# Kernel tuning notes

Hardware: AMD Instinct MI355X
Metric: run time of the kernel (lower is better)

## Reference

```python
import jax, jax.numpy as jnp
import numpy as np

B = 4096
D1 = 2048   # APPEARANCE_DIM
D2 = 1024   # POSE_DIM
DF = 8192   # FUSED_DIM
LN_EPS = 1e-5
L2_EPS = 1e-12


def setup_inputs() -> dict:
    key = jax.random.key(0)
    ks = jax.random.split(key, 6)
    x = jax.random.normal(ks[0], (B, D1), dtype=jnp.float32)
    y = jax.random.normal(ks[1], (B, D2), dtype=jnp.float32)
    h1 = jax.random.randint(ks[2], (D1,), 0, DF, dtype=jnp.int32)
    h2 = jax.random.randint(ks[3], (D2,), 0, DF, dtype=jnp.int32)
    s1 = (2 * jax.random.randint(ks[4], (D1,), 0, 2) - 1).astype(jnp.float32)
    s2 = (2 * jax.random.randint(ks[5], (D2,), 0, 2) - 1).astype(jnp.float32)
    gamma = jnp.ones((DF,), dtype=jnp.float32)
    beta = jnp.zeros((DF,), dtype=jnp.float32)
    return {"x": x, "y": y, "s1": s1, "s2": s2, "gamma": gamma,
            "beta": beta, "h1": h1, "h2": h2}


def count_sketch(v, h, s, out_dim):
    # v: [B, Din], h: [Din] int indices into out_dim, s: [Din] +-1 signs
    # single vectorized scatter-add along the feature axis
    return jnp.zeros((v.shape[0], out_dim), v.dtype).at[:, h].add(v * s)


def reference(x, y, s1, s2, gamma, beta, h1, h2):
    x_sk = count_sketch(x, h1, s1, DF)          # [B, DF]
    y_sk = count_sketch(y, h2, s2, DF)          # [B, DF]
    # circular convolution via FFT
    fused = jnp.fft.ifft(jnp.fft.fft(x_sk, axis=1) * jnp.fft.fft(y_sk, axis=1),
                         axis=1).real           # [B, DF]
    # LayerNorm over last dim
    mu = jnp.mean(fused, axis=-1, keepdims=True)
    var = jnp.mean(jnp.square(fused - mu), axis=-1, keepdims=True)
    normed = (fused - mu) * jax.lax.rsqrt(var + LN_EPS) * gamma + beta
    # F.normalize(p=2, dim=1)
    nrm = jnp.linalg.norm(normed, axis=1, keepdims=True)
    return normed / jnp.maximum(nrm, L2_EPS)
```

## Files before the change

kernel.cpp:

```cpp
#include <hip/hip_runtime.h>
#include <math.h>

#define DF 8192
#define NT 512

#define PH(i) ((i) ^ (((i) >> 5) & 14))

__device__ __forceinline__ float2 cmul(float2 a, float2 b) {
    return make_float2(a.x * b.x - a.y * b.y, a.x * b.y + a.y * b.x);
}
__device__ __forceinline__ float2 cadd(float2 a, float2 b) { return make_float2(a.x + b.x, a.y + b.y); }
__device__ __forceinline__ float2 csub(float2 a, float2 b) { return make_float2(a.x - b.x, a.y - b.y); }
__device__ __forceinline__ float2 cmuli(float2 a) { return make_float2(-a.y, a.x); }

#define RT_C 0.92387953251128674f
#define RT_S 0.38268343236508977f
#define RT_H 0.70710678118654752f

__device__ __forceinline__ float2 rootF(int j) {
    switch (j & 7) {
        case 0:  return make_float2( 1.f,   0.f  );
        case 1:  return make_float2( RT_C, -RT_S );
        case 2:  return make_float2( RT_H, -RT_H );
        case 3:  return make_float2( RT_S, -RT_C );
        case 4:  return make_float2( 0.f,  -1.f  );
        case 5:  return make_float2(-RT_S, -RT_C );
        case 6:  return make_float2(-RT_H, -RT_H );
        default: return make_float2(-RT_C, -RT_S );
    }
}
__device__ __forceinline__ float2 rootI(int j) {
    float2 r = rootF(j);
    return make_float2(r.x, -r.y);
}

__device__ __forceinline__ int brev9(int x) { return (int)(__brev((unsigned)x) >> 23); }

__device__ __forceinline__ void fft16_dif(float2 v[16], float2 wb) {
    const float2 wb2 = cmul(wb, wb);
    const float2 wb4 = cmul(wb2, wb2);
    const float2 wb8 = cmul(wb4, wb4);
    #pragma unroll
    for (int m = 0; m < 8; ++m) {
        float2 W = cmul(wb, rootF(m));
        float2 a = v[m], b = v[m + 8];
        v[m] = cadd(a, b);
        v[m + 8] = cmul(csub(a, b), W);
    }
    #pragma unroll
    for (int g = 0; g < 2; ++g)
        #pragma unroll
        for (int m = 0; m < 4; ++m) {
            int i = 8 * g + m;
            float2 W = cmul(wb2, rootF(2 * m));
            float2 a = v[i], b = v[i + 4];
            v[i] = cadd(a, b);
            v[i + 4] = cmul(csub(a, b), W);
        }
    #pragma unroll
    for (int g = 0; g < 4; ++g)
        #pragma unroll
        for (int m = 0; m < 2; ++m) {
            int i = 4 * g + m;
            float2 W = cmul(wb4, rootF(4 * m));
            float2 a = v[i], b = v[i + 2];
            v[i] = cadd(a, b);
            v[i + 2] = cmul(csub(a, b), W);
        }
    #pragma unroll
    for (int g = 0; g < 8; ++g) {
        int i = 2 * g;
        float2 a = v[i], b = v[i + 1];
        v[i] = cadd(a, b);
        v[i + 1] = cmul(csub(a, b), wb8);
    }
}

__device__ __forceinline__ void bf_dit(float2& a, float2& b, float2 W) {
    float2 bw = cmul(b, W);
    float2 ta = a;
    a = cadd(ta, bw);
    b = csub(ta, bw);
}
__device__ __forceinline__ void bf_dit1(float2& a, float2& b) {
    float2 tb = b, ta = a;
    a = cadd(ta, tb);
    b = csub(ta, tb);
}
__device__ __forceinline__ void bf_diti(float2& a, float2& b) {
    float2 bw = cmuli(b);
    float2 ta = a;
    a = cadd(ta, bw);
    b = csub(ta, bw);
}

__device__ __forceinline__ void fft8_dit(float2 v[8], float2 wq) {
    const float2 wq2 = cmul(wq, wq);
    const float2 wq4 = cmul(wq2, wq2);
    #pragma unroll
    for (int g = 0; g < 4; ++g) bf_dit(v[2 * g], v[2 * g + 1], wq4);
    #pragma unroll
    for (int g = 0; g < 2; ++g) {
        bf_dit(v[4 * g],     v[4 * g + 2], wq2);
        bf_dit(v[4 * g + 1], v[4 * g + 3], cmuli(wq2));
    }
    bf_dit(v[0], v[4], wq);
    bf_dit(v[1], v[5], cmul(wq, make_float2(RT_H, RT_H)));
    bf_dit(v[2], v[6], cmuli(wq));
    bf_dit(v[3], v[7], cmul(wq, make_float2(-RT_H, RT_H)));
}

__device__ __forceinline__ void fft8_dit1(float2 v[8]) {
    #pragma unroll
    for (int g = 0; g < 4; ++g) bf_dit1(v[2 * g], v[2 * g + 1]);
    #pragma unroll
    for (int g = 0; g < 2; ++g) {
        bf_dit1(v[4 * g],     v[4 * g + 2]);
        bf_diti(v[4 * g + 1], v[4 * g + 3]);
    }
    bf_dit1(v[0], v[4]);
    bf_dit (v[1], v[5], make_float2(RT_H, RT_H));
    bf_diti(v[2], v[6]);
    bf_dit (v[3], v[7], make_float2(-RT_H, RT_H));
}

__global__ __launch_bounds__(NT, 4)
void mcb3(const float* __restrict__ x, const float* __restrict__ y,
          const float* __restrict__ s1, const float* __restrict__ s2,
          const float* __restrict__ gamma, const float* __restrict__ beta,
          const int* __restrict__ h1, const int* __restrict__ h2,
          float* __restrict__ out)
{
    __shared__ float2 z[DF];
    const int t = threadIdx.x;
    const int row = blockIdx.x;

    #pragma unroll
    for (int m = 0; m < 16; ++m) z[t + NT * m] = make_float2(0.f, 0.f);
    __syncthreads();

    {
        const float4* x4  = (const float4*)(x + (size_t)row * 2048);
        const float4* s14 = (const float4*)s1;
        const int4*   h14 = (const int4*)h1;
        float4 xv = x4[t], sv = s14[t];
        int4 hv = h14[t];
        atomicAdd(&z[PH(hv.x)].x, xv.x * sv.x);
        atomicAdd(&z[PH(hv.y)].x, xv.y * sv.y);
        atomicAdd(&z[PH(hv.z)].x, xv.z * sv.z);
        atomicAdd(&z[PH(hv.w)].x, xv.w * sv.w);
        const float2* y2  = (const float2*)(y + (size_t)row * 1024);
        const float2* s22 = (const float2*)s2;
        const int2*   h22 = (const int2*)h2;
        float2 yv = y2[t], tv = s22[t];
        int2 hw = h22[t];
        atomicAdd(&z[PH(hw.x)].y, yv.x * tv.x);
        atomicAdd(&z[PH(hw.y)].y, yv.y * tv.y);
    }
    __syncthreads();

    float sn, cs;

    {
        float2 v[16];
        #pragma unroll
        for (int m = 0; m < 16; ++m) v[m] = z[PH(t + 512 * m)];
        __sincosf(-(float)M_PI / 4096.f * (float)t, &sn, &cs);
        fft16_dif(v, make_float2(cs, sn));
        #pragma unroll
        for (int m = 0; m < 16; ++m) z[PH(t + 512 * m)] = v[m];
    }
    __syncthreads();

    {
        const int lo = t & 31, hi = t >> 5;
        float2 v[16];
        #pragma unroll
        for (int m = 0; m < 16; ++m) v[m] = z[PH(lo + 32 * m + 512 * hi)];
        __sincosf(-(float)M_PI / 256.f * (float)lo, &sn, &cs);
        fft16_dif(v, make_float2(cs, sn));
        #pragma unroll
        for (int m = 0; m < 16; ++m) z[PH(lo + 32 * m + 512 * hi)] = v[m];
    }
    __syncthreads();

    {
        const int lo = t & 1, hi = t >> 1;
        float2 v[16];
        #pragma unroll
        for (int m = 0; m < 16; ++m) v[m] = z[PH(lo + 2 * m + 32 * hi)];
        __sincosf(-(float)M_PI / 16.f * (float)lo, &sn, &cs);
        fft16_dif(v, make_float2(cs, sn));
        #pragma unroll
        for (int m = 0; m < 16; ++m) z[PH(lo + 2 * m + 32 * hi)] = v[m];
    }
    __syncthreads();

    float2 u8[8];
    {
        const int R  = brev9(t);
        const int tp = brev9((512 - R) & 511);
        float2 a[8], b[8], pa[8], pb[8];
        #pragma unroll
        for (int m = 0; m < 8; ++m) {
            float4 q = *(const float4*)&z[PH(16 * t + 2 * m)];
            a[m] = make_float2(q.x, q.y);  b[m] = make_float2(q.z, q.w);
            float4 qp = *(const float4*)&z[PH(16 * tp + 2 * (7 - m))];
            pa[m] = make_float2(qp.x, qp.y); pb[m] = make_float2(qp.z, qp.w);
        }
        #pragma unroll
        for (int m = 0; m < 8; ++m) {
            float2 ta = a[m],  tb = b[m];
            a[m] = cadd(ta, tb);  b[m] = csub(ta, tb);
            ta = pa[m]; tb = pb[m];
            pa[m] = cadd(ta, tb); pb[m] = csub(ta, tb);
        }
        if (t == 0) {
            float2 ca[8], cb[8];
            #pragma unroll
            for (int m = 0; m < 8; ++m) { ca[m] = a[m]; cb[m] = b[m]; }
            const int tbl[8] = {0, 1, 3, 2, 7, 6, 5, 4};
            #pragma unroll
            for (int m = 0; m < 8; ++m) {
                if (m == 0) { pa[0] = cb[0]; pb[0] = ca[0]; }
                else        { pa[m] = ca[tbl[m]]; pb[m] = cb[tbl[m]]; }
            }
        }
        __sincosf((float)M_PI / 4096.f * (float)R, &sn, &cs);
        const float2 wR = make_float2(cs, sn);
        const float invN = 1.f / 8192.f;
        const int MB[8] = {0, 4, 2, 6, 1, 5, 3, 7};
        #pragma unroll
        for (int m = 0; m < 8; ++m) {
            float2 A = a[m], B = b[m], A2 = pa[m], B2 = pb[m];
            float X1r = 0.5f * (A.x + B2.x), X1i = 0.5f * (A.y - B2.y);
            float Y1r = 0.5f * (A.y + B2.y), Y1i = 0.5f * (B2.x - A.x);
            float2 P1 = make_float2((X1r * Y1r - X1i * Y1i) * invN,
                                    (X1r * Y1i + X1i * Y1r) * invN);
            float X2r = 0.5f * (B.x + A2.x), X2i = 0.5f * (B.y - A2.y);
            float Y2r = 0.5f * (B.y + A2.y), Y2i = 0.5f * (A2.x - B.x);
            float2 P2 = make_float2((X2r * Y2r - X2i * Y2i) * invN,
                                    (X2r * Y2i + X2i * Y2r) * invN);
            float2 S = cadd(P1, P2);
            float2 D = csub(P1, P2);
            float2 Dw = cmul(D, cmul(wR, rootI(MB[m])));
            u8[m] = make_float2(S.x - Dw.y, S.y + Dw.x);
        }
        fft8_dit1(u8);
        __syncthreads();
        #pragma unroll
        for (int g = 0; g < 4; ++g) {
            *(float4*)&z[PH(8 * t + 2 * g)] =
                make_float4(u8[2 * g].x, u8[2 * g].y, u8[2 * g + 1].x, u8[2 * g + 1].y);
        }
    }
    __syncthreads();

    {
        const int lo = t & 7, hi = t >> 3;
        #pragma unroll
        for (int m = 0; m < 8; ++m) u8[m] = z[PH(lo + 8 * m + 64 * hi)];
        __sincosf((float)M_PI / 32.f * (float)lo, &sn, &cs);
        fft8_dit(u8, make_float2(cs, sn));
        #pragma unroll
        for (int m = 0; m < 8; ++m) z[PH(lo + 8 * m + 64 * hi)] = u8[m];
    }
    __syncthreads();

    {
        const int lo = t & 63, hi = t >> 6;
        #pragma unroll
        for (int m = 0; m < 8; ++m) u8[m] = z[PH(lo + 64 * m + 512 * hi)];
        __sincosf((float)M_PI / 256.f * (float)lo, &sn, &cs);
        fft8_dit(u8, make_float2(cs, sn));
        #pragma unroll
        for (int m = 0; m < 8; ++m) z[PH(lo + 64 * m + 512 * hi)] = u8[m];
    }
    __syncthreads();

    #pragma unroll
    for (int m = 0; m < 8; ++m) u8[m] = z[PH(t + 512 * m)];
    __sincosf((float)M_PI / 2048.f * (float)t, &sn, &cs);
    fft8_dit(u8, make_float2(cs, sn));

    float lsum = 0.f, lsq = 0.f;
    #pragma unroll
    for (int m = 0; m < 8; ++m) {
        lsum += u8[m].x + u8[m].y;
        lsq  += u8[m].x * u8[m].x + u8[m].y * u8[m].y;
    }
    #pragma unroll
    for (int k = 32; k >= 1; k >>= 1) { lsum += __shfl_xor(lsum, k); lsq += __shfl_xor(lsq, k); }
    const int wid = t >> 6, lane = t & 63;
    __syncthreads();
    if (lane == 0) z[wid] = make_float2(lsum, lsq);
    __syncthreads();
    float tsum = 0.f, tsq = 0.f;
    #pragma unroll
    for (int w = 0; w < 8; ++w) { tsum += z[w].x; tsq += z[w].y; }
    const float mu   = tsum * (1.f / (float)DF);
    const float var  = tsq * (1.f / (float)DF) - mu * mu;
    const float rstd = rsqrtf(var + 1e-5f);

    const float2* g2  = (const float2*)gamma;
    const float2* bt2 = (const float2*)beta;
    float2 nv[8];
    float lsq2 = 0.f;
    #pragma unroll
    for (int m = 0; m < 8; ++m) {
        int i = t + 512 * m;
        float2 g = g2[i], bb = bt2[i];
        float ne = (u8[m].x - mu) * rstd * g.x + bb.x;
        float no = (u8[m].y - mu) * rstd * g.y + bb.y;
        nv[m] = make_float2(ne, no);
        lsq2 += ne * ne + no * no;
    }
    #pragma unroll
    for (int k = 32; k >= 1; k >>= 1) lsq2 += __shfl_xor(lsq2, k);
    if (lane == 0) z[8 + wid].x = lsq2;
    __syncthreads();
    float t2 = 0.f;
    #pragma unroll
    for (int w = 0; w < 8; ++w) t2 += z[8 + w].x;
    const float inv = 1.f / fmaxf(sqrtf(t2), 1e-12f);

    float2* o2 = (float2*)(out + (size_t)row * DF);
    #pragma unroll
    for (int m = 0; m < 8; ++m)
        o2[t + 512 * m] = make_float2(nv[m].x * inv, nv[m].y * inv);
}

extern "C" void kernel_launch(void* const* d_in, const int* in_sizes, int n_in,
                              void* d_out, int out_size, void* d_ws, size_t ws_size,
                              hipStream_t stream) {
    const float* x     = (const float*)d_in[0];
    const float* y     = (const float*)d_in[1];
    const float* s1    = (const float*)d_in[2];
    const float* s2    = (const float*)d_in[3];
    const float* gamma = (const float*)d_in[4];
    const float* beta  = (const float*)d_in[5];
    const int*   h1    = (const int*)d_in[6];
    const int*   h2    = (const int*)d_in[7];
    float* out = (float*)d_out;

    hipLaunchKernelGGL(mcb3, dim3(4096), dim3(NT), 0, stream,
                       x, y, s1, s2, gamma, beta, h1, h2, out);
}
```

Measured before the change: 180.3 us.

## Process two rows per block to amortize twiddles and syncs

Each block now handles two batch rows with a 128 KB shared buffer, interleaving the two FFT pipelines so twiddle computation, index math, hash/sign loads and barriers are shared across rows. This doubles the independent work per thread, which raises ILP and halves the grid. In exchange, shared memory and register use per block double and launch bounds drop to 2 blocks per CU, which may reduce occupancy and latency hiding.

```diff
diff --git a/kernel.cpp b/kernel.cpp
--- a/kernel.cpp
+++ b/kernel.cpp
@@ -36,298 +36,303 @@
 
 __device__ __forceinline__ int brev9(int x) { return (int)(__brev((unsigned)x) >> 23); }
 
-__device__ __forceinline__ void fft16_dif(float2 v[16], float2 wb) {
+__device__ __forceinline__ void bf_dif_dual(float2& a0, float2& b0, float2& a1, float2& b1, float2 W) {
+    float2 d0 = csub(a0, b0); a0 = cadd(a0, b0); b0 = cmul(d0, W);
+    float2 d1 = csub(a1, b1); a1 = cadd(a1, b1); b1 = cmul(d1, W);
+}
+__device__ __forceinline__ void bf_dit_dual(float2& a0, float2& b0, float2& a1, float2& b1, float2 W) {
+    float2 w0 = cmul(b0, W); b0 = csub(a0, w0); a0 = cadd(a0, w0);
+    float2 w1 = cmul(b1, W); b1 = csub(a1, w1); a1 = cadd(a1, w1);
+}
+__device__ __forceinline__ void bf_dit1_dual(float2& a0, float2& b0, float2& a1, float2& b1) {
+    float2 t0 = b0; b0 = csub(a0, t0); a0 = cadd(a0, t0);
+    float2 t1 = b1; b1 = csub(a1, t1); a1 = cadd(a1, t1);
+}
+__device__ __forceinline__ void bf_diti_dual(float2& a0, float2& b0, float2& a1, float2& b1) {
+    float2 w0 = cmuli(b0); b0 = csub(a0, w0); a0 = cadd(a0, w0);
+    float2 w1 = cmuli(b1); b1 = csub(a1, w1); a1 = cadd(a1, w1);
+}
+
+__device__ __forceinline__ void fft16_dif_dual(float2 va[16], float2 vb[16], float2 wb) {
     const float2 wb2 = cmul(wb, wb);
     const float2 wb4 = cmul(wb2, wb2);
     const float2 wb8 = cmul(wb4, wb4);
     #pragma unroll
     for (int m = 0; m < 8; ++m) {
         float2 W = cmul(wb, rootF(m));
-        float2 a = v[m], b = v[m + 8];
-        v[m] = cadd(a, b);
-        v[m + 8] = cmul(csub(a, b), W);
-    }
-    #pragma unroll
-    for (int g = 0; g < 2; ++g)
-        #pragma unroll
-        for (int m = 0; m < 4; ++m) {
-            int i = 8 * g + m;
-            float2 W = cmul(wb2, rootF(2 * m));
-            float2 a = v[i], b = v[i + 4];
-            v[i] = cadd(a, b);
-            v[i + 4] = cmul(csub(a, b), W);
+        bf_dif_dual(va[m], va[m + 8], vb[m], vb[m + 8], W);
+    }
+    #pragma unroll
+    for (int m = 0; m < 4; ++m) {
+        float2 W = cmul(wb2, rootF(2 * m));
+        bf_dif_dual(va[m],     va[m + 4],  vb[m],     vb[m + 4],  W);
+        bf_dif_dual(va[8 + m], va[12 + m], vb[8 + m], vb[12 + m], W);
+    }
+    #pragma unroll
+    for (int m = 0; m < 2; ++m) {
+        float2 W = cmul(wb4, rootF(4 * m));
+        #pragma unroll
+        for (int g = 0; g < 4; ++g) {
+            int i = 4 * g + m;
+            bf_dif_dual(va[i], va[i + 2], vb[i], vb[i + 2], W);
         }
-    #pragma unroll
-    for (int g = 0; g < 4; ++g)
-        #pragma unroll
-        for (int m = 0; m < 2; ++m) {
-            int i = 4 * g + m;
-            float2 W = cmul(wb4, rootF(4 * m));
-            float2 a = v[i], b = v[i + 2];
-            v[i] = cadd(a, b);
-            v[i + 2] = cmul(csub(a, b), W);
-        }
-    #pragma unroll
-    for (int g = 0; g < 8; ++g) {
-        int i = 2 * g;
-        float2 a = v[i], b = v[i + 1];
-        v[i] = cadd(a, b);
-        v[i + 1] = cmul(csub(a, b), wb8);
-    }
-}
-
-__device__ __forceinline__ void bf_dit(float2& a, float2& b, float2 W) {
-    float2 bw = cmul(b, W);
-    float2 ta = a;
-    a = cadd(ta, bw);
-    b = csub(ta, bw);
-}
-__device__ __forceinline__ void bf_dit1(float2& a, float2& b) {
-    float2 tb = b, ta = a;
-    a = cadd(ta, tb);
-    b = csub(ta, tb);
-}
-__device__ __forceinline__ void bf_diti(float2& a, float2& b) {
-    float2 bw = cmuli(b);
-    float2 ta = a;
-    a = cadd(ta, bw);
-    b = csub(ta, bw);
-}
-
-__device__ __forceinline__ void fft8_dit(float2 v[8], float2 wq) {
+    }
+    #pragma unroll
+    for (int g = 0; g < 8; ++g)
+        bf_dif_dual(va[2 * g], va[2 * g + 1], vb[2 * g], vb[2 * g + 1], wb8);
+}
+
+__device__ __forceinline__ void fft8_dit_dual(float2 va[8], float2 vb[8], float2 wq) {
     const float2 wq2 = cmul(wq, wq);
     const float2 wq4 = cmul(wq2, wq2);
     #pragma unroll
-    for (int g = 0; g < 4; ++g) bf_dit(v[2 * g], v[2 * g + 1], wq4);
+    for (int g = 0; g < 4; ++g) bf_dit_dual(va[2 * g], va[2 * g + 1], vb[2 * g], vb[2 * g + 1], wq4);
+    const float2 iwq2 = cmuli(wq2);
     #pragma unroll
     for (int g = 0; g < 2; ++g) {
-        bf_dit(v[4 * g],     v[4 * g + 2], wq2);
-        bf_dit(v[4 * g + 1], v[4 * g + 3], cmuli(wq2));
-    }
-    bf_dit(v[0], v[4], wq);
-    bf_dit(v[1], v[5], cmul(wq, make_float2(RT_H, RT_H)));
-    bf_dit(v[2], v[6], cmuli(wq));
-    bf_dit(v[3], v[7], cmul(wq, make_float2(-RT_H, RT_H)));
-}
-
-__device__ __forceinline__ void fft8_dit1(float2 v[8]) {
-    #pragma unroll
-    for (int g = 0; g < 4; ++g) bf_dit1(v[2 * g], v[2 * g + 1]);
+        bf_dit_dual(va[4 * g],     va[4 * g + 2], vb[4 * g],     vb[4 * g + 2], wq2);
+        bf_dit_dual(va[4 * g + 1], va[4 * g + 3], vb[4 * g + 1], vb[4 * g + 3], iwq2);
+    }
+    bf_dit_dual(va[0], va[4], vb[0], vb[4], wq);
+    bf_dit_dual(va[1], va[5], vb[1], vb[5], cmul(wq, make_float2(RT_H, RT_H)));
+    bf_dit_dual(va[2], va[6], vb[2], vb[6], cmuli(wq));
+    bf_dit_dual(va[3], va[7], vb[3], vb[7], cmul(wq, make_float2(-RT_H, RT_H)));
+}
+__device__ __forceinline__ void fft8_dit1_dual(float2 va[8], float2 vb[8]) {
+    #pragma unroll
+    for (int g = 0; g < 4; ++g) bf_dit1_dual(va[2 * g], va[2 * g + 1], vb[2 * g], vb[2 * g + 1]);
     #pragma unroll
     for (int g = 0; g < 2; ++g) {
-        bf_dit1(v[4 * g],     v[4 * g + 2]);
-        bf_diti(v[4 * g + 1], v[4 * g + 3]);
-    }
-    bf_dit1(v[0], v[4]);
-    bf_dit (v[1], v[5], make_float2(RT_H, RT_H));
-    bf_diti(v[2], v[6]);
-    bf_dit (v[3], v[7], make_float2(-RT_H, RT_H));
-}
-
-__global__ __launch_bounds__(NT, 4)
-void mcb3(const float* __restrict__ x, const float* __restrict__ y,
+        bf_dit1_dual(va[4 * g],     va[4 * g + 2], vb[4 * g],     vb[4 * g + 2]);
+        bf_diti_dual(va[4 * g + 1], va[4 * g + 3], vb[4 * g + 1], vb[4 * g + 3]);
+    }
+    bf_dit1_dual(va[0], va[4], vb[0], vb[4]);
+    bf_dit_dual (va[1], va[5], vb[1], vb[5], make_float2(RT_H, RT_H));
+    bf_diti_dual(va[2], va[6], vb[2], vb[6]);
+    bf_dit_dual (va[3], va[7], vb[3], vb[7], make_float2(-RT_H, RT_H));
+}
+
+__device__ __forceinline__ float2 mega_combine(float2 A, float2 B, float2 PA, float2 PB,
+                                               float2 W, float invN) {
+    float X1r = 0.5f * (A.x + PB.x), X1i = 0.5f * (A.y - PB.y);
+    float Y1r = 0.5f * (A.y + PB.y), Y1i = 0.5f * (PB.x - A.x);
+    float2 P1 = make_float2((X1r * Y1r - X1i * Y1i) * invN, (X1r * Y1i + X1i * Y1r) * invN);
+    float X2r = 0.5f * (B.x + PA.x), X2i = 0.5f * (B.y - PA.y);
+    float Y2r = 0.5f * (B.y + PA.y), Y2i = 0.5f * (PA.x - B.x);
+    float2 P2 = make_float2((X2r * Y2r - X2i * Y2i) * invN, (X2r * Y2i + X2i * Y2r) * invN);
+    float2 S = cadd(P1, P2);
+    float2 D = csub(P1, P2);
+    float2 Dw = cmul(D, W);
+    return make_float2(S.x - Dw.y, S.y + Dw.x);
+}
+
+__global__ __launch_bounds__(NT, 2)
+void mcb4(const float* __restrict__ x, const float* __restrict__ y,
           const float* __restrict__ s1, const float* __restrict__ s2,
           const float* __restrict__ gamma, const float* __restrict__ beta,
           const int* __restrict__ h1, const int* __restrict__ h2,
           float* __restrict__ out)
 {
-    __shared__ float2 z[DF];
+    __shared__ float2 z[2 * DF];
+    float2* z0 = z;
+    float2* z1 = z + DF;
     const int t = threadIdx.x;
-    const int row = blockIdx.x;
-
-    #pragma unroll
-    for (int m = 0; m < 16; ++m) z[t + NT * m] = make_float2(0.f, 0.f);
-    __syncthreads();
-
-    {
-        const float4* x4  = (const float4*)(x + (size_t)row * 2048);
-        const float4* s14 = (const float4*)s1;
-        const int4*   h14 = (const int4*)h1;
-        float4 xv = x4[t], sv = s14[t];
-        int4 hv = h14[t];
-        atomicAdd(&z[PH(hv.x)].x, xv.x * sv.x);
-        atomicAdd(&z[PH(hv.y)].x, xv.y * sv.y);
-        atomicAdd(&z[PH(hv.z)].x, xv.z * sv.z);
-        atomicAdd(&z[PH(hv.w)].x, xv.w * sv.w);
-        const float2* y2  = (const float2*)(y + (size_t)row * 1024);
-        const float2* s22 = (const float2*)s2;
-        const int2*   h22 = (const int2*)h2;
-        float2 yv = y2[t], tv = s22[t];
-        int2 hw = h22[t];
-        atomicAdd(&z[PH(hw.x)].y, yv.x * tv.x);
-        atomicAdd(&z[PH(hw.y)].y, yv.y * tv.y);
+    const int rA = blockIdx.x * 2, rB = rA + 1;
+
+    {
+        float4* z4 = (float4*)z;
+        #pragma unroll
+        for (int m = 0; m < 16; ++m) z4[t + NT * m] = make_float4(0.f, 0.f, 0.f, 0.f);
+    }
+    __syncthreads();
+
+    {
+        float4 sv = ((const float4*)s1)[t];
+        int4   hv = ((const int4*)h1)[t];
+        float4 xa = ((const float4*)(x + (size_t)rA * 2048))[t];
+        float4 xb = ((const float4*)(x + (size_t)rB * 2048))[t];
+        int p0 = PH(hv.x), p1 = PH(hv.y), p2 = PH(hv.z), p3 = PH(hv.w);
+        atomicAdd(&z0[p0].x, xa.x * sv.x);  atomicAdd(&z1[p0].x, xb.x * sv.x);
+        atomicAdd(&z0[p1].x, xa.y * sv.y);  atomicAdd(&z1[p1].x, xb.y * sv.y);
+        atomicAdd(&z0[p2].x, xa.z * sv.z);  atomicAdd(&z1[p2].x, xb.z * sv.z);
+        atomicAdd(&z0[p3].x, xa.w * sv.w);  atomicAdd(&z1[p3].x, xb.w * sv.w);
+        float2 tv = ((const float2*)s2)[t];
+        int2   hw = ((const int2*)h2)[t];
+        float2 ya = ((const float2*)(y + (size_t)rA * 1024))[t];
+        float2 yb = ((const float2*)(y + (size_t)rB * 1024))[t];
+        int q0 = PH(hw.x), q1 = PH(hw.y);
+        atomicAdd(&z0[q0].y, ya.x * tv.x);  atomicAdd(&z1[q0].y, yb.x * tv.x);
+        atomicAdd(&z0[q1].y, ya.y * tv.y);  atomicAdd(&z1[q1].y, yb.y * tv.y);
     }
     __syncthreads();
 
     float sn, cs;
-
-    {
-        float2 v[16];
-        #pragma unroll
-        for (int m = 0; m < 16; ++m) v[m] = z[PH(t + 512 * m)];
+    {
+        float2 va[16], vb[16];
+
+        #pragma unroll
+        for (int m = 0; m < 16; ++m) { int p = PH(t + 512 * m); va[m] = z0[p]; vb[m] = z1[p]; }
         __sincosf(-(float)M_PI / 4096.f * (float)t, &sn, &cs);
-        fft16_dif(v, make_float2(cs, sn));
-        #pragma unroll
-        for (int m = 0; m < 16; ++m) z[PH(t + 512 * m)] = v[m];
-    }
-    __syncthreads();
-
-    {
-        const int lo = t & 31, hi = t >> 5;
-        float2 v[16];
-        #pragma unroll
-        for (int m = 0; m < 16; ++m) v[m] = z[PH(lo + 32 * m + 512 * hi)];
-        __sincosf(-(float)M_PI / 256.f * (float)lo, &sn, &cs);
-        fft16_dif(v, make_float2(cs, sn));
-        #pragma unroll
-        for (int m = 0; m < 16; ++m) z[PH(lo + 32 * m + 512 * hi)] = v[m];
-    }
-    __syncthreads();
-
-    {
-        const int lo = t & 1, hi = t >> 1;
-        float2 v[16];
-        #pragma unroll
-        for (int m = 0; m < 16; ++m) v[m] = z[PH(lo + 2 * m + 32 * hi)];
-        __sincosf(-(float)M_PI / 16.f * (float)lo, &sn, &cs);
-        fft16_dif(v, make_float2(cs, sn));
-        #pragma unroll
-        for (int m = 0; m < 16; ++m) z[PH(lo + 2 * m + 32 * hi)] = v[m];
-    }
-    __syncthreads();
-
-    float2 u8[8];
+        fft16_dif_dual(va, vb, make_float2(cs, sn));
+        #pragma unroll
+        for (int m = 0; m < 16; ++m) { int p = PH(t + 512 * m); z0[p] = va[m]; z1[p] = vb[m]; }
+        __syncthreads();
+
+        {
+            const int lo = t & 31, hi = t >> 5;
+            #pragma unroll
+            for (int m = 0; m < 16; ++m) { int p = PH(lo + 32 * m + 512 * hi); va[m] = z0[p]; vb[m] = z1[p]; }
+            __sincosf(-(float)M_PI / 256.f * (float)lo, &sn, &cs);
+            fft16_dif_dual(va, vb, make_float2(cs, sn));
+            #pragma unroll
+            for (int m = 0; m < 16; ++m) { int p = PH(lo + 32 * m + 512 * hi); z0[p] = va[m]; z1[p] = vb[m]; }
+        }
+        __syncthreads();
+
+        {
+            const int lo = t & 1, hi = t >> 1;
+            #pragma unroll
+            for (int m = 0; m < 16; ++m) { int p = PH(lo + 2 * m + 32 * hi); va[m] = z0[p]; vb[m] = z1[p]; }
+            __sincosf(-(float)M_PI / 16.f * (float)lo, &sn, &cs);
+            fft16_dif_dual(va, vb, make_float2(cs, sn));
+            #pragma unroll
+            for (int m = 0; m < 16; ++m) { int p = PH(lo + 2 * m + 32 * hi); z0[p] = va[m]; z1[p] = vb[m]; }
+        }
+        __syncthreads();
+    }
+
+    float2 uA[8], uB[8];
     {
         const int R  = brev9(t);
         const int tp = brev9((512 - R) & 511);
-        float2 a[8], b[8], pa[8], pb[8];
-        #pragma unroll
-        for (int m = 0; m < 8; ++m) {
-            float4 q = *(const float4*)&z[PH(16 * t + 2 * m)];
-            a[m] = make_float2(q.x, q.y);  b[m] = make_float2(q.z, q.w);
-            float4 qp = *(const float4*)&z[PH(16 * tp + 2 * (7 - m))];
-            pa[m] = make_float2(qp.x, qp.y); pb[m] = make_float2(qp.z, qp.w);
-        }
-        #pragma unroll
-        for (int m = 0; m < 8; ++m) {
-            float2 ta = a[m],  tb = b[m];
-            a[m] = cadd(ta, tb);  b[m] = csub(ta, tb);
-            ta = pa[m]; tb = pb[m];
-            pa[m] = cadd(ta, tb); pb[m] = csub(ta, tb);
-        }
-        if (t == 0) {
-            float2 ca[8], cb[8];
-            #pragma unroll
-            for (int m = 0; m < 8; ++m) { ca[m] = a[m]; cb[m] = b[m]; }
-            const int tbl[8] = {0, 1, 3, 2, 7, 6, 5, 4};
-            #pragma unroll
-            for (int m = 0; m < 8; ++m) {
-                if (m == 0) { pa[0] = cb[0]; pb[0] = ca[0]; }
-                else        { pa[m] = ca[tbl[m]]; pb[m] = cb[tbl[m]]; }
-            }
-        }
         __sincosf((float)M_PI / 4096.f * (float)R, &sn, &cs);
         const float2 wR = make_float2(cs, sn);
         const float invN = 1.f / 8192.f;
-        const int MB[8] = {0, 4, 2, 6, 1, 5, 3, 7};
+        const int MB[8]   = {0, 4, 2, 6, 1, 5, 3, 7};
+        const int TBL2[8] = {0, 2, 6, 4, 14, 12, 10, 8};
         #pragma unroll
         for (int m = 0; m < 8; ++m) {
-            float2 A = a[m], B = b[m], A2 = pa[m], B2 = pb[m];
-            float X1r = 0.5f * (A.x + B2.x), X1i = 0.5f * (A.y - B2.y);
-            float Y1r = 0.5f * (A.y + B2.y), Y1i = 0.5f * (B2.x - A.x);
-            float2 P1 = make_float2((X1r * Y1r - X1i * Y1i) * invN,
-                                    (X1r * Y1i + X1i * Y1r) * invN);
-            float X2r = 0.5f * (B.x + A2.x), X2i = 0.5f * (B.y - A2.y);
-            float Y2r = 0.5f * (B.y + A2.y), Y2i = 0.5f * (A2.x - B.x);
-            float2 P2 = make_float2((X2r * Y2r - X2i * Y2i) * invN,
-                                    (X2r * Y2i + X2i * Y2r) * invN);
-            float2 S = cadd(P1, P2);
-            float2 D = csub(P1, P2);
-            float2 Dw = cmul(D, cmul(wR, rootI(MB[m])));
-            u8[m] = make_float2(S.x - Dw.y, S.y + Dw.x);
+            int own = PH(16 * t + 2 * m);
+            int pp  = (t == 0) ? PH(TBL2[m]) : PH(16 * tp + 2 * (7 - m));
+            float4 qa = *(const float4*)&z0[own];
+            float4 qb = *(const float4*)&z1[own];
+            float4 ra = *(const float4*)&z0[pp];
+            float4 rb = *(const float4*)&z1[pp];
+            float2 A0  = make_float2(qa.x + qa.z, qa.y + qa.w);
+            float2 B0  = make_float2(qa.x - qa.z, qa.y - qa.w);
+            float2 A1  = make_float2(qb.x + qb.z, qb.y + qb.w);
+            float2 B1  = make_float2(qb.x - qb.z, qb.y - qb.w);
+            float2 PA0 = make_float2(ra.x + ra.z, ra.y + ra.w);
+            float2 PB0 = make_float2(ra.x - ra.z, ra.y - ra.w);
+            float2 PA1 = make_float2(rb.x + rb.z, rb.y + rb.w);
+            float2 PB1 = make_float2(rb.x - rb.z, rb.y - rb.w);
+            if (m == 0) {
+                if (t == 0) {
+                    float2 s0 = PA0; PA0 = PB0; PB0 = s0;
+                    float2 s1_ = PA1; PA1 = PB1; PB1 = s1_;
+                }
+            }
+            float2 W = cmul(wR, rootI(MB[m]));
+            uA[m] = mega_combine(A0, B0, PA0, PB0, W, invN);
+            uB[m] = mega_combine(A1, B1, PA1, PB1, W, invN);
         }
-        fft8_dit1(u8);
-        __syncthreads();
-        #pragma unroll
-        for (int g = 0; g < 4; ++g) {
-            *(float4*)&z[PH(8 * t + 2 * g)] =
-                make_float4(u8[2 * g].x, u8[2 * g].y, u8[2 * g + 1].x, u8[2 * g + 1].y);
-        }
+        fft8_dit1_dual(uA, uB);
+    }
+    __syncthreads();
+    #pragma unroll
+    for (int g = 0; g < 4; ++g) {
+        int p = PH(8 * t + 2 * g);
+        *(float4*)&z0[p] = make_float4(uA[2 * g].x, uA[2 * g].y, uA[2 * g + 1].x, uA[2 * g + 1].y);
+        *(float4*)&z1[p] = make_float4(uB[2 * g].x, uB[2 * g].y, uB[2 * g + 1].x, uB[2 * g + 1].y);
     }
     __syncthreads();
 
     {
         const int lo = t & 7, hi = t >> 3;
         #pragma unroll
-        for (int m = 0; m < 8; ++m) u8[m] = z[PH(lo + 8 * m + 64 * hi)];
+        for (int m = 0; m < 8; ++m) { int p = PH(lo + 8 * m + 64 * hi); uA[m] = z0[p]; uB[m] = z1[p]; }
         __sincosf((float)M_PI / 32.f * (float)lo, &sn, &cs);
-        fft8_dit(u8, make_float2(cs, sn));
-        #pragma unroll
-        for (int m = 0; m < 8; ++m) z[PH(lo + 8 * m + 64 * hi)] = u8[m];
+        fft8_dit_dual(uA, uB, make_float2(cs, sn));
+        #pragma unroll
+        for (int m = 0; m < 8; ++m) { int p = PH(lo + 8 * m + 64 * hi); z0[p] = uA[m]; z1[p] = uB[m]; }
     }
     __syncthreads();
 
     {
         const int lo = t & 63, hi = t >> 6;
         #pragma unroll
-        for (int m = 0; m < 8; ++m) u8[m] = z[PH(lo + 64 * m + 512 * hi)];
+        for (int m = 0; m < 8; ++m) { int p = PH(lo + 64 * m + 512 * hi); uA[m] = z0[p]; uB[m] = z1[p]; }
         __sincosf((float)M_PI / 256.f * (float)lo, &sn, &cs);
-        fft8_dit(u8, make_float2(cs, sn));
-        #pragma unroll
-        for (int m = 0; m < 8; ++m) z[PH(lo + 64 * m + 512 * hi)] = u8[m];
-    }
-    __syncthreads();
-
-    #pragma unroll
-    for (int m = 0; m < 8; ++m) u8[m] = z[PH(t + 512 * m)];
+        fft8_dit_dual(uA, uB, make_float2(cs, sn));
+        #pragma unroll
+        for (int m = 0; m < 8; ++m) { int p = PH(lo + 64 * m + 512 * hi); z0[p] = uA[m]; z1[p] = uB[m]; }
+    }
+    __syncthreads();
+
+    #pragma unroll
+    for (int m = 0; m < 8; ++m) { int p = PH(t + 512 * m); uA[m] = z0[p]; uB[m] = z1[p]; }
     __sincosf((float)M_PI / 2048.f * (float)t, &sn, &cs);
-    fft8_dit(u8, make_float2(cs, sn));
-
-    float lsum = 0.f, lsq = 0.f;
+    fft8_dit_dual(uA, uB, make_float2(cs, sn));
+
+    float lsA = 0.f, lqA = 0.f, lsB = 0.f, lqB = 0.f;
     #pragma unroll
     for (int m = 0; m < 8; ++m) {
-        lsum += u8[m].x + u8[m].y;
-        lsq  += u8[m].x * u8[m].x + u8[m].y * u8[m].y;
-    }
-    #pragma unroll
-    for (int k = 32; k >= 1; k >>= 1) { lsum += __shfl_xor(lsum, k); lsq += __shfl_xor(lsq, k); }
+        lsA += uA[m].x + uA[m].y;  lqA += uA[m].x * uA[m].x + uA[m].y * uA[m].y;
+        lsB += uB[m].x + uB[m].y;  lqB += uB[m].x * uB[m].x + uB[m].y * uB[m].y;
+    }
+    #pragma unroll
+    for (int k = 32; k >= 1; k >>= 1) {
+        lsA += __shfl_xor(lsA, k);  lqA += __shfl_xor(lqA, k);
+        lsB += __shfl_xor(lsB, k);  lqB += __shfl_xor(lqB, k);
+    }
     const int wid = t >> 6, lane = t & 63;
     __syncthreads();
-    if (lane == 0) z[wid] = make_float2(lsum, lsq);
-    __syncthreads();
-    float tsum = 0.f, tsq = 0.f;
-    #pragma unroll
-    for (int w = 0; w < 8; ++w) { tsum += z[w].x; tsq += z[w].y; }
-    const float mu   = tsum * (1.f / (float)DF);
-    const float var  = tsq * (1.f / (float)DF) - mu * mu;
-    const float rstd = rsqrtf(var + 1e-5f);
+    if (lane == 0) { z0[wid] = make_float2(lsA, lqA); z1[wid] = make_float2(lsB, lqB); }
+    __syncthreads();
+    float tsA = 0.f, tqA = 0.f, tsB = 0.f, tqB = 0.f;
+    #pragma unroll
+    for (int w = 0; w < 8; ++w) {
+        tsA += z0[w].x; tqA += z0[w].y;
+        tsB += z1[w].x; tqB += z1[w].y;
+    }
+    const float muA = tsA * (1.f / (float)DF);
+    const float muB = tsB * (1.f / (float)DF);
+    const float rstdA = rsqrtf(tqA * (1.f / (float)DF) - muA * muA + 1e-5f);
+    const float rstdB = rsqrtf(tqB * (1.f / (float)DF) - muB * muB + 1e-5f);
 
     const float2* g2  = (const float2*)gamma;
     const float2* bt2 = (const float2*)beta;
-    float2 nv[8];
-    float lsq2 = 0.f;
+    float l2A = 0.f, l2B = 0.f;
     #pragma unroll
     for (int m = 0; m < 8; ++m) {
         int i = t + 512 * m;
         float2 g = g2[i], bb = bt2[i];
-        float ne = (u8[m].x - mu) * rstd * g.x + bb.x;
-        float no = (u8[m].y - mu) * rstd * g.y + bb.y;
-        nv[m] = make_float2(ne, no);
-        lsq2 += ne * ne + no * no;
-    }
-    #pragma unroll
-    for (int k = 32; k >= 1; k >>= 1) lsq2 += __shfl_xor(lsq2, k);
-    if (lane == 0) z[8 + wid].x = lsq2;
-    __syncthreads();
-    float t2 = 0.f;
-    #pragma unroll
-    for (int w = 0; w < 8; ++w) t2 += z[8 + w].x;
-    const float inv = 1.f / fmaxf(sqrtf(t2), 1e-12f);
-
-    float2* o2 = (float2*)(out + (size_t)row * DF);
-    #pragma unroll
-    for (int m = 0; m < 8; ++m)
-        o2[t + 512 * m] = make_float2(nv[m].x * inv, nv[m].y * inv);
+        float aE = (uA[m].x - muA) * rstdA * g.x + bb.x;
+        float aO = (uA[m].y - muA) * rstdA * g.y + bb.y;
+        float bE = (uB[m].x - muB) * rstdB * g.x + bb.x;
+        float bO = (uB[m].y - muB) * rstdB * g.y + bb.y;
+        uA[m] = make_float2(aE, aO);
+        uB[m] = make_float2(bE, bO);
+        l2A += aE * aE + aO * aO;
+        l2B += bE * bE + bO * bO;
+    }
+    #pragma unroll
+    for (int k = 32; k >= 1; k >>= 1) { l2A += __shfl_xor(l2A, k); l2B += __shfl_xor(l2B, k); }
+    if (lane == 0) z0[8 + wid] = make_float2(l2A, l2B);
+    __syncthreads();
+    float t2A = 0.f, t2B = 0.f;
+    #pragma unroll
+    for (int w = 0; w < 8; ++w) { t2A += z0[8 + w].x; t2B += z0[8 + w].y; }
+    const float invA = 1.f / fmaxf(sqrtf(t2A), 1e-12f);
+    const float invB = 1.f / fmaxf(sqrtf(t2B), 1e-12f);
+
+    float2* oA = (float2*)(out + (size_t)rA * DF);
+    float2* oB = (float2*)(out + (size_t)rB * DF);
+    #pragma unroll
+    for (int m = 0; m < 8; ++m) {
+        oA[t + 512 * m] = make_float2(uA[m].x * invA, uA[m].y * invA);
+        oB[t + 512 * m] = make_float2(uB[m].x * invB, uB[m].y * invB);
+    }
 }
 
 extern "C" void kernel_launch(void* const* d_in, const int* in_sizes, int n_in,
@@ -343,6 +348,6 @@
     const int*   h2    = (const int*)d_in[7];
     float* out = (float*)d_out;
 
-    hipLaunchKernelGGL(mcb3, dim3(4096), dim3(NT), 0, stream,
+    hipLaunchKernelGGL(mcb4, dim3(2048), dim3(NT), 0, stream,
                        x, y, s1, s2, gamma, beta, h1, h2, out);
 }
```

Result: slower. 211.3 us (+17.2%).

## Restructure FFT passes into wave-local stages with wave-level sync instead of block barriers

Applied to the files above, without the earlier changes.

Reorganizes the forward FFT middle stages so each wavefront owns a contiguous 1024-element chunk (radix-8 plus radix-16 plus radix-4 sub-stages). This lets block-wide __syncthreads be replaced by s_waitcnt wave-level waits, and the inverse FFT middle stages get the same treatment. The pair-combine step now reads partner values directly from LDS inside the loop rather than preloading them, which lowers register pressure. The swizzle also widens to reduce bank conflicts. Relying on lgkmcnt waits alone for intra-wave LDS ordering is riskier than full barriers.

```diff
diff --git a/kernel.cpp b/kernel.cpp
--- a/kernel.cpp
+++ b/kernel.cpp
@@ -4,14 +4,17 @@
 #define DF 8192
 #define NT 512
 
-#define PH(i) ((i) ^ (((i) >> 5) & 14))
+#define SW(i) ((i) ^ (((i) >> 5) & 30))
+
+#define WAVE_SYNC asm volatile("s_waitcnt lgkmcnt(0)" ::: "memory")
 
 __device__ __forceinline__ float2 cmul(float2 a, float2 b) {
     return make_float2(a.x * b.x - a.y * b.y, a.x * b.y + a.y * b.x);
 }
 __device__ __forceinline__ float2 cadd(float2 a, float2 b) { return make_float2(a.x + b.x, a.y + b.y); }
 __device__ __forceinline__ float2 csub(float2 a, float2 b) { return make_float2(a.x - b.x, a.y - b.y); }
-__device__ __forceinline__ float2 cmuli(float2 a) { return make_float2(-a.y, a.x); }
+__device__ __forceinline__ float2 cmuli(float2 a)  { return make_float2(-a.y, a.x); }
+__device__ __forceinline__ float2 cmulmi(float2 a) { return make_float2(a.y, -a.x); }
 
 #define RT_C 0.92387953251128674f
 #define RT_S 0.38268343236508977f
@@ -36,46 +39,21 @@
 
 __device__ __forceinline__ int brev9(int x) { return (int)(__brev((unsigned)x) >> 23); }
 
-__device__ __forceinline__ void fft16_dif(float2 v[16], float2 wb) {
-    const float2 wb2 = cmul(wb, wb);
-    const float2 wb4 = cmul(wb2, wb2);
-    const float2 wb8 = cmul(wb4, wb4);
-    #pragma unroll
-    for (int m = 0; m < 8; ++m) {
-        float2 W = cmul(wb, rootF(m));
-        float2 a = v[m], b = v[m + 8];
-        v[m] = cadd(a, b);
-        v[m + 8] = cmul(csub(a, b), W);
-    }
-    #pragma unroll
-    for (int g = 0; g < 2; ++g)
-        #pragma unroll
-        for (int m = 0; m < 4; ++m) {
-            int i = 8 * g + m;
-            float2 W = cmul(wb2, rootF(2 * m));
-            float2 a = v[i], b = v[i + 4];
-            v[i] = cadd(a, b);
-            v[i + 4] = cmul(csub(a, b), W);
-        }
-    #pragma unroll
-    for (int g = 0; g < 4; ++g)
-        #pragma unroll
-        for (int m = 0; m < 2; ++m) {
-            int i = 4 * g + m;
-            float2 W = cmul(wb4, rootF(4 * m));
-            float2 a = v[i], b = v[i + 2];
-            v[i] = cadd(a, b);
-            v[i + 2] = cmul(csub(a, b), W);
-        }
-    #pragma unroll
-    for (int g = 0; g < 8; ++g) {
-        int i = 2 * g;
-        float2 a = v[i], b = v[i + 1];
-        v[i] = cadd(a, b);
-        v[i + 1] = cmul(csub(a, b), wb8);
-    }
-}
-
+__device__ __forceinline__ void bf_dif(float2& a, float2& b, float2 W) {
+    float2 d = csub(a, b);
+    a = cadd(a, b);
+    b = cmul(d, W);
+}
+__device__ __forceinline__ void bf_dif1(float2& a, float2& b) {
+    float2 d = csub(a, b);
+    a = cadd(a, b);
+    b = d;
+}
+__device__ __forceinline__ void bf_difmi(float2& a, float2& b) {
+    float2 d = csub(a, b);
+    a = cadd(a, b);
+    b = cmulmi(d);
+}
 __device__ __forceinline__ void bf_dit(float2& a, float2& b, float2 W) {
     float2 bw = cmul(b, W);
     float2 ta = a;
@@ -94,22 +72,62 @@
     b = csub(ta, bw);
 }
 
+__device__ __forceinline__ void fft16_dif(float2 v[16], float2 wb) {
+    const float2 wb2 = cmul(wb, wb);
+    const float2 wb4 = cmul(wb2, wb2);
+    const float2 wb8 = cmul(wb4, wb4);
+    #pragma unroll
+    for (int m = 0; m < 8; ++m) bf_dif(v[m], v[m + 8], cmul(wb, rootF(m)));
+    #pragma unroll
+    for (int m = 0; m < 4; ++m) {
+        float2 W = cmul(wb2, rootF(2 * m));
+        bf_dif(v[m],     v[m + 4],  W);
+        bf_dif(v[8 + m], v[12 + m], W);
+    }
+    #pragma unroll
+    for (int g = 0; g < 4; ++g)
+        #pragma unroll
+        for (int m = 0; m < 2; ++m)
+            bf_dif(v[4 * g + m], v[4 * g + m + 2], cmul(wb4, rootF(4 * m)));
+    #pragma unroll
+    for (int g = 0; g < 8; ++g) bf_dif(v[2 * g], v[2 * g + 1], wb8);
+}
+
+__device__ __forceinline__ void fft16_dif3(float2 v[16], float2 wA) {
+    const float2 wA2 = cmul(wA, wA);
+    const float2 wA4 = cmul(wA2, wA2);
+    #pragma unroll
+    for (int m = 0; m < 4; ++m) {
+        float2 W = cmul(wA, rootF(2 * m));
+        bf_dif(v[m],     v[m + 4],  W);
+        bf_dif(v[8 + m], v[12 + m], W);
+    }
+    #pragma unroll
+    for (int a = 0; a < 4; ++a)
+        #pragma unroll
+        for (int q = 0; q < 2; ++q)
+            bf_dif(v[4 * a + q], v[4 * a + q + 2], cmul(wA2, rootF(4 * q)));
+    #pragma unroll
+    for (int c = 0; c < 8; ++c)
+        bf_dif(v[2 * c], v[2 * c + 1], wA4);
+}
+
 __device__ __forceinline__ void fft8_dit(float2 v[8], float2 wq) {
     const float2 wq2 = cmul(wq, wq);
     const float2 wq4 = cmul(wq2, wq2);
     #pragma unroll
     for (int g = 0; g < 4; ++g) bf_dit(v[2 * g], v[2 * g + 1], wq4);
+    const float2 iwq2 = cmuli(wq2);
     #pragma unroll
     for (int g = 0; g < 2; ++g) {
         bf_dit(v[4 * g],     v[4 * g + 2], wq2);
-        bf_dit(v[4 * g + 1], v[4 * g + 3], cmuli(wq2));
+        bf_dit(v[4 * g + 1], v[4 * g + 3], iwq2);
     }
     bf_dit(v[0], v[4], wq);
     bf_dit(v[1], v[5], cmul(wq, make_float2(RT_H, RT_H)));
     bf_dit(v[2], v[6], cmuli(wq));
     bf_dit(v[3], v[7], cmul(wq, make_float2(-RT_H, RT_H)));
 }
-
 __device__ __forceinline__ void fft8_dit1(float2 v[8]) {
     #pragma unroll
     for (int g = 0; g < 4; ++g) bf_dit1(v[2 * g], v[2 * g + 1]);
@@ -124,210 +142,210 @@
     bf_dit (v[3], v[7], make_float2(-RT_H, RT_H));
 }
 
+__device__ __forceinline__ float2 mega_combine(float2 A, float2 B, float2 PA, float2 PB,
+                                               float2 W, float invN) {
+    float X1r = 0.5f * (A.x + PB.x), X1i = 0.5f * (A.y - PB.y);
+    float Y1r = 0.5f * (A.y + PB.y), Y1i = 0.5f * (PB.x - A.x);
+    float2 P1 = make_float2((X1r * Y1r - X1i * Y1i) * invN, (X1r * Y1i + X1i * Y1r) * invN);
+    float X2r = 0.5f * (B.x + PA.x), X2i = 0.5f * (B.y - PA.y);
+    float Y2r = 0.5f * (B.y + PA.y), Y2i = 0.5f * (PA.x - B.x);
+    float2 P2 = make_float2((X2r * Y2r - X2i * Y2i) * invN, (X2r * Y2i + X2i * Y2r) * invN);
+    float2 S = cadd(P1, P2);
+    float2 D = csub(P1, P2);
+    float2 Dw = cmul(D, W);
+    return make_float2(S.x - Dw.y, S.y + Dw.x);
+}
+
 __global__ __launch_bounds__(NT, 4)
-void mcb3(const float* __restrict__ x, const float* __restrict__ y,
+void mcb6(const float* __restrict__ x, const float* __restrict__ y,
           const float* __restrict__ s1, const float* __restrict__ s2,
           const float* __restrict__ gamma, const float* __restrict__ beta,
           const int* __restrict__ h1, const int* __restrict__ h2,
           float* __restrict__ out)
 {
     __shared__ float2 z[DF];
-    const int t = threadIdx.x;
+    const int t  = threadIdx.x;
+    const int l  = t & 63;
+    const int wv = t >> 6;
     const int row = blockIdx.x;
 
-    #pragma unroll
-    for (int m = 0; m < 16; ++m) z[t + NT * m] = make_float2(0.f, 0.f);
-    __syncthreads();
-
-    {
-        const float4* x4  = (const float4*)(x + (size_t)row * 2048);
-        const float4* s14 = (const float4*)s1;
-        const int4*   h14 = (const int4*)h1;
-        float4 xv = x4[t], sv = s14[t];
-        int4 hv = h14[t];
-        atomicAdd(&z[PH(hv.x)].x, xv.x * sv.x);
-        atomicAdd(&z[PH(hv.y)].x, xv.y * sv.y);
-        atomicAdd(&z[PH(hv.z)].x, xv.z * sv.z);
-        atomicAdd(&z[PH(hv.w)].x, xv.w * sv.w);
-        const float2* y2  = (const float2*)(y + (size_t)row * 1024);
-        const float2* s22 = (const float2*)s2;
-        const int2*   h22 = (const int2*)h2;
-        float2 yv = y2[t], tv = s22[t];
-        int2 hw = h22[t];
-        atomicAdd(&z[PH(hw.x)].y, yv.x * tv.x);
-        atomicAdd(&z[PH(hw.y)].y, yv.y * tv.y);
+    {
+        float4* z4 = (float4*)z;
+        #pragma unroll
+        for (int m = 0; m < 8; ++m) z4[t + NT * m] = make_float4(0.f, 0.f, 0.f, 0.f);
+    }
+    __syncthreads();
+
+    {
+        float4 xv = ((const float4*)(x + (size_t)row * 2048))[t];
+        float4 sv = ((const float4*)s1)[t];
+        int4   hv = ((const int4*)h1)[t];
+        atomicAdd(&z[SW(hv.x)].x, xv.x * sv.x);
+        atomicAdd(&z[SW(hv.y)].x, xv.y * sv.y);
+        atomicAdd(&z[SW(hv.z)].x, xv.z * sv.z);
+        atomicAdd(&z[SW(hv.w)].x, xv.w * sv.w);
+        float2 yv = ((const float2*)(y + (size_t)row * 1024))[t];
+        float2 tv = ((const float2*)s2)[t];
+        int2   hw = ((const int2*)h2)[t];
+        atomicAdd(&z[SW(hw.x)].y, yv.x * tv.x);
+        atomicAdd(&z[SW(hw.y)].y, yv.y * tv.y);
     }
     __syncthreads();
 
     float sn, cs;
-
-    {
-        float2 v[16];
-        #pragma unroll
-        for (int m = 0; m < 16; ++m) v[m] = z[PH(t + 512 * m)];
-        __sincosf(-(float)M_PI / 4096.f * (float)t, &sn, &cs);
+    float2 v[16];
+
+    #pragma unroll
+    for (int m = 0; m < 16; ++m) v[m] = z[SW(t + 512 * m)];
+    __sincosf(-(float)M_PI / 4096.f * (float)t, &sn, &cs);
+    fft16_dif(v, make_float2(cs, sn));
+    #pragma unroll
+    for (int m = 0; m < 16; ++m) z[SW(t + 512 * m)] = v[m];
+    __syncthreads();
+
+    const int cb = wv << 10;
+
+    #pragma unroll
+    for (int m = 0; m < 16; ++m) v[m] = z[SW(cb + l + 64 * m)];
+    __sincosf(-(float)M_PI / 256.f * (float)l, &sn, &cs);
+    fft16_dif3(v, make_float2(cs, sn));
+    #pragma unroll
+    for (int m = 0; m < 16; ++m) z[SW(cb + l + 64 * m)] = v[m];
+    WAVE_SYNC;
+
+    {
+        const int b = cb + (l & 3) + ((l >> 2) << 6);
+        #pragma unroll
+        for (int m = 0; m < 16; ++m) v[m] = z[SW(b + 4 * m)];
+        __sincosf(-(float)M_PI / 32.f * (float)(l & 3), &sn, &cs);
         fft16_dif(v, make_float2(cs, sn));
         #pragma unroll
-        for (int m = 0; m < 16; ++m) z[PH(t + 512 * m)] = v[m];
-    }
-    __syncthreads();
-
-    {
-        const int lo = t & 31, hi = t >> 5;
-        float2 v[16];
-        #pragma unroll
-        for (int m = 0; m < 16; ++m) v[m] = z[PH(lo + 32 * m + 512 * hi)];
-        __sincosf(-(float)M_PI / 256.f * (float)lo, &sn, &cs);
-        fft16_dif(v, make_float2(cs, sn));
-        #pragma unroll
-        for (int m = 0; m < 16; ++m) z[PH(lo + 32 * m + 512 * hi)] = v[m];
-    }
-    __syncthreads();
-
-    {
-        const int lo = t & 1, hi = t >> 1;
-        float2 v[16];
-        #pragma unroll
-        for (int m = 0; m < 16; ++m) v[m] = z[PH(lo + 2 * m + 32 * hi)];
-        __sincosf(-(float)M_PI / 16.f * (float)lo, &sn, &cs);
-        fft16_dif(v, make_float2(cs, sn));
-        #pragma unroll
-        for (int m = 0; m < 16; ++m) z[PH(lo + 2 * m + 32 * hi)] = v[m];
-    }
-    __syncthreads();
-
-    float2 u8[8];
+        for (int m = 0; m < 16; ++m) z[SW(b + 4 * m)] = v[m];
+    }
+    WAVE_SYNC;
+
+    {
+        const int b = cb + 16 * l;
+        #pragma unroll
+        for (int c = 0; c < 8; ++c) {
+            float4 q = *(const float4*)&z[SW(b + 2 * c)];
+            v[2 * c]     = make_float2(q.x, q.y);
+            v[2 * c + 1] = make_float2(q.z, q.w);
+        }
+        #pragma unroll
+        for (int a = 0; a < 4; ++a) {
+            bf_dif1 (v[4 * a],     v[4 * a + 2]);
+            bf_difmi(v[4 * a + 1], v[4 * a + 3]);
+        }
+        #pragma unroll
+        for (int c = 0; c < 8; ++c) bf_dif1(v[2 * c], v[2 * c + 1]);
+        #pragma unroll
+        for (int c = 0; c < 8; ++c)
+            *(float4*)&z[SW(b + 2 * c)] =
+                make_float4(v[2 * c].x, v[2 * c].y, v[2 * c + 1].x, v[2 * c + 1].y);
+    }
+    __syncthreads();
+
+    float2 u[8];
     {
         const int R  = brev9(t);
-        const int tp = brev9((512 - R) & 511);
-        float2 a[8], b[8], pa[8], pb[8];
-        #pragma unroll
-        for (int m = 0; m < 8; ++m) {
-            float4 q = *(const float4*)&z[PH(16 * t + 2 * m)];
-            a[m] = make_float2(q.x, q.y);  b[m] = make_float2(q.z, q.w);
-            float4 qp = *(const float4*)&z[PH(16 * tp + 2 * (7 - m))];
-            pa[m] = make_float2(qp.x, qp.y); pb[m] = make_float2(qp.z, qp.w);
-        }
-        #pragma unroll
-        for (int m = 0; m < 8; ++m) {
-            float2 ta = a[m],  tb = b[m];
-            a[m] = cadd(ta, tb);  b[m] = csub(ta, tb);
-            ta = pa[m]; tb = pb[m];
-            pa[m] = cadd(ta, tb); pb[m] = csub(ta, tb);
-        }
-        if (t == 0) {
-            float2 ca[8], cb[8];
-            #pragma unroll
-            for (int m = 0; m < 8; ++m) { ca[m] = a[m]; cb[m] = b[m]; }
-            const int tbl[8] = {0, 1, 3, 2, 7, 6, 5, 4};
-            #pragma unroll
-            for (int m = 0; m < 8; ++m) {
-                if (m == 0) { pa[0] = cb[0]; pb[0] = ca[0]; }
-                else        { pa[m] = ca[tbl[m]]; pb[m] = cb[tbl[m]]; }
-            }
-        }
+        const int tp = (R == 0) ? 0 : brev9(512 - R);
         __sincosf((float)M_PI / 4096.f * (float)R, &sn, &cs);
         const float2 wR = make_float2(cs, sn);
         const float invN = 1.f / 8192.f;
-        const int MB[8] = {0, 4, 2, 6, 1, 5, 3, 7};
-        #pragma unroll
-        for (int m = 0; m < 8; ++m) {
-            float2 A = a[m], B = b[m], A2 = pa[m], B2 = pb[m];
-            float X1r = 0.5f * (A.x + B2.x), X1i = 0.5f * (A.y - B2.y);
-            float Y1r = 0.5f * (A.y + B2.y), Y1i = 0.5f * (B2.x - A.x);
-            float2 P1 = make_float2((X1r * Y1r - X1i * Y1i) * invN,
-                                    (X1r * Y1i + X1i * Y1r) * invN);
-            float X2r = 0.5f * (B.x + A2.x), X2i = 0.5f * (B.y - A2.y);
-            float Y2r = 0.5f * (B.y + A2.y), Y2i = 0.5f * (A2.x - B.x);
-            float2 P2 = make_float2((X2r * Y2r - X2i * Y2i) * invN,
-                                    (X2r * Y2i + X2i * Y2r) * invN);
-            float2 S = cadd(P1, P2);
-            float2 D = csub(P1, P2);
-            float2 Dw = cmul(D, cmul(wR, rootI(MB[m])));
-            u8[m] = make_float2(S.x - Dw.y, S.y + Dw.x);
+        const int MB[8]  = {0, 4, 2, 6, 1, 5, 3, 7};
+        const int TBL[8] = {0, 1, 3, 2, 7, 6, 5, 4};
+        #pragma unroll
+        for (int g = 0; g < 8; ++g) {
+            int ps = (t == 0) ? (2 * TBL[g]) : (16 * tp + 2 * (7 - g));
+            float4 r = *(const float4*)&z[SW(ps)];
+            float2 PA = make_float2(r.x, r.y);
+            float2 PB = make_float2(r.z, r.w);
+            if (t == 0 && g == 0) { float2 s0 = PA; PA = PB; PB = s0; }
+            u[g] = mega_combine(v[2 * g], v[2 * g + 1], PA, PB,
+                                cmul(wR, rootI(MB[g])), invN);
         }
-        fft8_dit1(u8);
-        __syncthreads();
-        #pragma unroll
-        for (int g = 0; g < 4; ++g) {
-            *(float4*)&z[PH(8 * t + 2 * g)] =
-                make_float4(u8[2 * g].x, u8[2 * g].y, u8[2 * g + 1].x, u8[2 * g + 1].y);
-        }
-    }
-    __syncthreads();
-
-    {
-        const int lo = t & 7, hi = t >> 3;
-        #pragma unroll
-        for (int m = 0; m < 8; ++m) u8[m] = z[PH(lo + 8 * m + 64 * hi)];
-        __sincosf((float)M_PI / 32.f * (float)lo, &sn, &cs);
-        fft8_dit(u8, make_float2(cs, sn));
-        #pragma unroll
-        for (int m = 0; m < 8; ++m) z[PH(lo + 8 * m + 64 * hi)] = u8[m];
-    }
-    __syncthreads();
-
-    {
-        const int lo = t & 63, hi = t >> 6;
-        #pragma unroll
-        for (int m = 0; m < 8; ++m) u8[m] = z[PH(lo + 64 * m + 512 * hi)];
-        __sincosf((float)M_PI / 256.f * (float)lo, &sn, &cs);
-        fft8_dit(u8, make_float2(cs, sn));
-        #pragma unroll
-        for (int m = 0; m < 8; ++m) z[PH(lo + 64 * m + 512 * hi)] = u8[m];
-    }
-    __syncthreads();
-
-    #pragma unroll
-    for (int m = 0; m < 8; ++m) u8[m] = z[PH(t + 512 * m)];
+        fft8_dit1(u);
+    }
+    __syncthreads();
+    #pragma unroll
+    for (int c = 0; c < 4; ++c)
+        *(float4*)&z[SW(8 * t + 2 * c)] =
+            make_float4(u[2 * c].x, u[2 * c].y, u[2 * c + 1].x, u[2 * c + 1].y);
+    WAVE_SYNC;
+
+    const int b2 = wv << 9;
+
+    {
+        const int b = b2 + (l & 7) + ((l >> 3) << 6);
+        #pragma unroll
+        for (int m = 0; m < 8; ++m) u[m] = z[SW(b + 8 * m)];
+        __sincosf((float)M_PI / 32.f * (float)(l & 7), &sn, &cs);
+        fft8_dit(u, make_float2(cs, sn));
+        #pragma unroll
+        for (int m = 0; m < 8; ++m) z[SW(b + 8 * m)] = u[m];
+    }
+    WAVE_SYNC;
+
+    {
+        const int b = b2 + l;
+        #pragma unroll
+        for (int m = 0; m < 8; ++m) u[m] = z[SW(b + 64 * m)];
+        __sincosf((float)M_PI / 256.f * (float)l, &sn, &cs);
+        fft8_dit(u, make_float2(cs, sn));
+        #pragma unroll
+        for (int m = 0; m < 8; ++m) z[SW(b + 64 * m)] = u[m];
+    }
+    __syncthreads();
+
+    #pragma unroll
+    for (int m = 0; m < 8; ++m) u[m] = z[SW(t + 512 * m)];
     __sincosf((float)M_PI / 2048.f * (float)t, &sn, &cs);
-    fft8_dit(u8, make_float2(cs, sn));
+    fft8_dit(u, make_float2(cs, sn));
 
     float lsum = 0.f, lsq = 0.f;
     #pragma unroll
     for (int m = 0; m < 8; ++m) {
-        lsum += u8[m].x + u8[m].y;
-        lsq  += u8[m].x * u8[m].x + u8[m].y * u8[m].y;
+        lsum += u[m].x + u[m].y;
+        lsq  += u[m].x * u[m].x + u[m].y * u[m].y;
     }
     #pragma unroll
     for (int k = 32; k >= 1; k >>= 1) { lsum += __shfl_xor(lsum, k); lsq += __shfl_xor(lsq, k); }
-    const int wid = t >> 6, lane = t & 63;
-    __syncthreads();
-    if (lane == 0) z[wid] = make_float2(lsum, lsq);
+    __syncthreads();
+    if (l == 0) z[wv] = make_float2(lsum, lsq);
     __syncthreads();
     float tsum = 0.f, tsq = 0.f;
     #pragma unroll
-    for (int w = 0; w < 8; ++w) { tsum += z[w].x; tsq += z[w].y; }
+    for (int w2 = 0; w2 < 8; ++w2) { tsum += z[w2].x; tsq += z[w2].y; }
     const float mu   = tsum * (1.f / (float)DF);
     const float var  = tsq * (1.f / (float)DF) - mu * mu;
     const float rstd = rsqrtf(var + 1e-5f);
 
     const float2* g2  = (const float2*)gamma;
     const float2* bt2 = (const float2*)beta;
-    float2 nv[8];
     float lsq2 = 0.f;
     #pragma unroll
     for (int m = 0; m < 8; ++m) {
         int i = t + 512 * m;
         float2 g = g2[i], bb = bt2[i];
-        float ne = (u8[m].x - mu) * rstd * g.x + bb.x;
-        float no = (u8[m].y - mu) * rstd * g.y + bb.y;
-        nv[m] = make_float2(ne, no);
+        float ne = (u[m].x - mu) * rstd * g.x + bb.x;
+        float no = (u[m].y - mu) * rstd * g.y + bb.y;
+        u[m] = make_float2(ne, no);
         lsq2 += ne * ne + no * no;
     }
     #pragma unroll
     for (int k = 32; k >= 1; k >>= 1) lsq2 += __shfl_xor(lsq2, k);
-    if (lane == 0) z[8 + wid].x = lsq2;
+    if (l == 0) z[8 + wv].x = lsq2;
     __syncthreads();
     float t2 = 0.f;
     #pragma unroll
-    for (int w = 0; w < 8; ++w) t2 += z[8 + w].x;
+    for (int w2 = 0; w2 < 8; ++w2) t2 += z[8 + w2].x;
     const float inv = 1.f / fmaxf(sqrtf(t2), 1e-12f);
 
     float2* o2 = (float2*)(out + (size_t)row * DF);
     #pragma unroll
     for (int m = 0; m < 8; ++m)
-        o2[t + 512 * m] = make_float2(nv[m].x * inv, nv[m].y * inv);
+        o2[t + 512 * m] = make_float2(u[m].x * inv, u[m].y * inv);
 }
 
 extern "C" void kernel_launch(void* const* d_in, const int* in_sizes, int n_in,
@@ -343,6 +361,6 @@
     const int*   h2    = (const int*)d_in[7];
     float* out = (float*)d_out;
 
-    hipLaunchKernelGGL(mcb3, dim3(4096), dim3(NT), 0, stream,
+    hipLaunchKernelGGL(mcb6, dim3(4096), dim3(NT), 0, stream,
                        x, y, s1, s2, gamma, beta, h1, h2, out);
 }
```

After: 198.3 us. 1.1x slower.
